# Optimization experiments

Hardware: AMD Instinct MI355X
Metric: run time of the kernel (lower is better)

## Reference

```python
import jax, jax.numpy as jnp
import numpy as np

B = 16384
D = 64            # bottom_mlp_layers[-1] = embedding_dim
DENSE = 512
HIST = 50         # history length per row
C_CAMP = 1000     # num_collisions for campaign table (sqrt(1e6))
C_FEAT = 316      # num_collisions for 1e5-vocab tables
NQ_CAMP = 1000    # ceil(1e6/1000)
NQ_FEAT = 317     # ceil(1e5/316)
NFEAT = 7
N = NFEAT + 1 + 1 # sparse features + dense row
PROJ = 128


def setup_inputs() -> dict:
    key = jax.random.key(0)
    ks = jax.random.split(key, 20)
    inp = {
        'x': jax.random.normal(ks[0], (B, DENSE), jnp.float32),
        'hist_idx': jax.random.randint(ks[1], (B * HIST,), 0, 1000000),
        'hist_offsets': jnp.arange(B, dtype=jnp.int64) * HIST,
        'feat_idx': jax.random.randint(ks[2], (B, NFEAT), 0, 100000),
        # QR embedding tables (quotient, remainder)
        'Wq_c': jax.random.normal(ks[3], (NQ_CAMP, D), jnp.float32) * 0.05,
        'Wr_c': jax.random.normal(ks[4], (C_CAMP, D), jnp.float32) * 0.05,
        'Wq_f': jax.random.normal(ks[5], (NFEAT, NQ_FEAT, D), jnp.float32) * 0.05,
        'Wr_f': jax.random.normal(ks[6], (NFEAT, C_FEAT, D), jnp.float32) * 0.05,
        # bottom MLP: 512->512 relu 512->256 relu 256->64
        'W0': jax.random.normal(ks[7], (512, DENSE), jnp.float32) * 0.03,
        'b0': jnp.zeros((512,), jnp.float32),
        'W1': jax.random.normal(ks[8], (256, 512), jnp.float32) * 0.04,
        'b1': jnp.zeros((256,), jnp.float32),
        'W2': jax.random.normal(ks[9], (64, 256), jnp.float32) * 0.06,
        'b2': jnp.zeros((64,), jnp.float32),
        # projection: (D + (N^2-N)/2) -> PROJ ; 64 + 36 = 100
        'Wp': jax.random.normal(ks[10], (PROJ, D + (N * N - N) // 2), jnp.float32) * 0.1,
        'bp': jnp.zeros((PROJ,), jnp.float32),
    }
    return inp


def _forward(x, hist_idx, hist_offsets, feat_idx, Wq_c, Wr_c, Wq_f, Wr_f,
             W0, b0, W1, b1, W2, b2, Wp, bp):
    # bottom MLP
    h = jax.nn.relu(x @ W0.T + b0)
    h = jax.nn.relu(h @ W1.T + b1)
    dense = h @ W2.T + b2                                   # [B, D]

    # QR embedding bag (mode='mean', operation='mult') for history feature
    e = Wq_c[hist_idx // C_CAMP] * Wr_c[hist_idx % C_CAMP]  # [M, D]
    M = hist_idx.shape[0]
    seg = jnp.cumsum(jnp.zeros((M,), jnp.int32).at[hist_offsets].add(1)) - 1
    sums = jax.ops.segment_sum(e, seg, num_segments=B)      # [B, D]
    counts = jnp.diff(jnp.concatenate([hist_offsets, jnp.array([M], hist_offsets.dtype)]))
    hist_emb = sums / counts[:, None].astype(sums.dtype)

    # single-valued QR lookups (bag size 1 -> mean == lookup)
    t = jnp.arange(NFEAT)[None, :]
    fe = Wq_f[t, feat_idx // C_FEAT] * Wr_f[t, feat_idx % C_FEAT]  # [B, NFEAT, D]

    # pairwise dot interaction: upper triangle (offset=1) of T @ T^T
    T = jnp.concatenate([dense[:, None, :], hist_emb[:, None, :], fe], axis=1)  # [B, N, D]
    Z = jnp.einsum('bnd,bmd->bnm', T, T)
    row, col = np.triu_indices(N, k=1)
    Z_flat = Z[:, row, col]                                  # [B, (N^2-N)/2]

    combined = jnp.concatenate([dense, Z_flat], axis=1)
    return combined @ Wp.T + bp                              # [B, PROJ]


def reference(x, hist_idx, hist_offsets, feat_idx, Wq_c, Wr_c, Wq_f, Wr_f,
              W0, b0, W1, b1, W2, b2, Wp, bp):
    return _forward(x, hist_idx, hist_offsets, feat_idx, Wq_c, Wr_c, Wq_f, Wr_f,
                    W0, b0, W1, b1, W2, b2, Wp, bp)
```

## Files before the change

kernel.cpp:

```cpp
#include <hip/hip_runtime.h>
#include <hip/hip_bf16.h>
#include <stdint.h>

#define DENSE_D 512
#define HIDDEN1 512
#define HIDDEN2 256
#define EMB_D   64
#define NFEAT   7
#define NROWS   9
#define NPAIRS  36
#define COMB    100
#define KPROJ   128
#define PROJ    128
#define C_CAMP  1000
#define C_FEAT  316
#define NQ_FEAT 317
#define TROWS   16

typedef __attribute__((ext_vector_type(8)))  __bf16 bf16x8;
typedef __attribute__((ext_vector_type(8)))  unsigned short ushort8;
typedef __attribute__((ext_vector_type(4)))  float  facc4;

#define GLD_LDS16(gp, lp) __builtin_amdgcn_global_load_lds( \
    (__attribute__((address_space(1))) void*)(gp), \
    (__attribute__((address_space(3))) void*)(lp), 16, 0, 0)

__device__ inline unsigned short f2bf(float f) {
    __hip_bfloat16 h = __float2bfloat16(f);
    return *reinterpret_cast<unsigned short*>(&h);
}
__device__ inline float blo(unsigned int u) { return __uint_as_float(u << 16); }
__device__ inline float bhi(unsigned int u) { return __uint_as_float(u & 0xffff0000u); }

template<int BM, int BN, int BK, bool RELU>
__global__ __launch_bounds__(256)
void gemm16(const unsigned short* __restrict__ A,
            const unsigned short* __restrict__ W,
            const float* __restrict__ bias,
            unsigned short* __restrict__ Cout,
            int M, int N, int K)
{
    constexpr int THREADS = 256;
    constexpr int MREP    = BM / 16;
    constexpr int NREP    = BN / (4 * 16);
    constexpr int SUB     = BK / 32;
    constexpr int ACH     = BM * BK / 8;
    constexpr int BCH     = BN * BK / 8;

    __shared__ __align__(16) unsigned short Asm[BK / 8][BM][8];
    __shared__ __align__(16) unsigned short Bsm[BK / 8][BN][8];

    const int tid  = threadIdx.x;
    const int lane = tid & 63;
    const int wave = tid >> 6;
    const int row0 = blockIdx.x * BM;
    const int col0 = blockIdx.y * BN;
    const int fr   = lane & 15;
    const int fk   = lane >> 4;

    facc4 acc[MREP][NREP] = {};

    for (int k0 = 0; k0 < K; k0 += BK) {
        #pragma unroll
        for (int it = 0; it < ACH / THREADS; ++it) {
            const int p  = it * THREADS + tid;
            const int r  = p & (BM - 1);
            const int kc = p / BM;
            GLD_LDS16(A + (size_t)(row0 + r) * K + k0 + kc * 8,
                      (&Asm[0][0][0]) + (size_t)p * 8);
        }
        #pragma unroll
        for (int it = 0; it < BCH / THREADS; ++it) {
            const int p  = it * THREADS + tid;
            const int r  = p & (BN - 1);
            const int kc = p / BN;
            GLD_LDS16(W + (size_t)(col0 + r) * K + k0 + kc * 8,
                      (&Bsm[0][0][0]) + (size_t)p * 8);
        }
        __syncthreads();

        #pragma unroll
        for (int s = 0; s < SUB; ++s) {
            bf16x8 af[MREP], bw[NREP];
            #pragma unroll
            for (int m = 0; m < MREP; ++m)
                af[m] = *reinterpret_cast<const bf16x8*>(
                    &Asm[s * 4 + fk][m * 16 + fr][0]);
            #pragma unroll
            for (int n = 0; n < NREP; ++n)
                bw[n] = *reinterpret_cast<const bf16x8*>(
                    &Bsm[s * 4 + fk][wave * (NREP * 16) + n * 16 + fr][0]);
            #pragma unroll
            for (int m = 0; m < MREP; ++m)
                #pragma unroll
                for (int n = 0; n < NREP; ++n)
                    acc[m][n] = __builtin_amdgcn_mfma_f32_16x16x32_bf16(
                        af[m], bw[n], acc[m][n], 0, 0, 0);
        }
        __syncthreads();
    }

    #pragma unroll
    for (int n = 0; n < NREP; ++n) {
        const int col = col0 + wave * (NREP * 16) + n * 16 + fr;
        const float bv = bias[col];
        #pragma unroll
        for (int m = 0; m < MREP; ++m) {
            #pragma unroll
            for (int j = 0; j < 4; ++j) {
                const int row = row0 + m * 16 + fk * 4 + j;
                float v = acc[m][n][j] + bv;
                if (RELU) v = fmaxf(v, 0.f);
                Cout[(size_t)row * N + col] = f2bf(v);
            }
        }
    }
}

__device__ inline void cast_seg(const float* __restrict__ src,
                                unsigned short* __restrict__ dst,
                                int n4, int id, int stride)
{
    for (int i = id; i < n4; i += stride) {
        const float4 v = reinterpret_cast<const float4*>(src)[i];
        ushort4 o;
        o.x = f2bf(v.x); o.y = f2bf(v.y); o.z = f2bf(v.z); o.w = f2bf(v.w);
        reinterpret_cast<ushort4*>(dst)[i] = o;
    }
}

__global__ __launch_bounds__(256)
void prep_all(const float* __restrict__ x,
              const float* __restrict__ W0, const float* __restrict__ W1,
              const float* __restrict__ W2, const float* __restrict__ Wp,
              const float* __restrict__ Wq_c, const float* __restrict__ Wr_c,
              const float* __restrict__ Wq_f, const float* __restrict__ Wr_f,
              unsigned short* xb,
              unsigned short* w0b, unsigned short* w1b, unsigned short* w2b,
              unsigned short* wpb, unsigned short* qcb, unsigned short* rcb,
              unsigned short* qfb, unsigned short* rfb, int M)
{
    const int id = blockIdx.x * blockDim.x + threadIdx.x;
    const int stride = gridDim.x * blockDim.x;
    cast_seg(x,    xb,  M * DENSE_D / 4,         id, stride);
    cast_seg(W0,   w0b, HIDDEN1 * DENSE_D / 4,   id, stride);
    cast_seg(W1,   w1b, HIDDEN2 * HIDDEN1 / 4,   id, stride);
    cast_seg(W2,   w2b, EMB_D * HIDDEN2 / 4,     id, stride);
    cast_seg(Wq_c, qcb, C_CAMP * EMB_D / 4,      id, stride);
    cast_seg(Wr_c, rcb, C_CAMP * EMB_D / 4,      id, stride);
    cast_seg(Wq_f, qfb, NFEAT * NQ_FEAT * EMB_D / 4, id, stride);
    cast_seg(Wr_f, rfb, NFEAT * C_FEAT * EMB_D / 4,  id, stride);
    for (int i = id; i < PROJ * KPROJ; i += stride) {
        const int r = i >> 7, c = i & 127;
        wpb[i] = (c < COMB) ? f2bf(Wp[r * COMB + c]) : (unsigned short)0;
    }
}

__global__ __launch_bounds__(256)
void tail_fused(const unsigned short* __restrict__ h1b,
                const unsigned short* __restrict__ w2b,
                const float* __restrict__ b2,
                const int* __restrict__ hist_idx,
                const int* __restrict__ hist_off,
                const int* __restrict__ feat_idx,
                const unsigned short* __restrict__ qcb,
                const unsigned short* __restrict__ rcb,
                const unsigned short* __restrict__ qfb,
                const unsigned short* __restrict__ rfb,
                const unsigned short* __restrict__ wpb,
                const float* __restrict__ bp,
                float* __restrict__ out,
                int B, int Mtot)
{
    const int r0   = blockIdx.x * TROWS;
    const int t    = threadIdx.x;
    const int lane = t & 63;
    const int wave = t >> 6;
    const int fr   = lane & 15;
    const int fk   = lane >> 4;

    __shared__ __align__(16) unsigned short T[TROWS][NROWS][68];
    __shared__ __align__(16) unsigned short combs[TROWS][136];

    {
        facc4 acc = {};
        const unsigned short* arow = h1b + (size_t)(r0 + fr) * HIDDEN2;
        const unsigned short* brow = w2b + (size_t)(wave * 16 + fr) * HIDDEN2;
        #pragma unroll
        for (int kw = 0; kw < 8; ++kw) {
            const bf16x8 af = *reinterpret_cast<const bf16x8*>(arow + kw * 32 + fk * 8);
            const bf16x8 bw = *reinterpret_cast<const bf16x8*>(brow + kw * 32 + fk * 8);
            acc = __builtin_amdgcn_mfma_f32_16x16x32_bf16(af, bw, acc, 0, 0, 0);
        }
        const int col = wave * 16 + fr;
        const float bv = b2[col];
        #pragma unroll
        for (int j = 0; j < 4; ++j) {
            const int row = fk * 4 + j;
            const unsigned short hv = f2bf(acc[j] + bv);
            T[row][0][col]  = hv;
            combs[row][col] = hv;
        }
    }

    for (int p = t; p < TROWS * 18; p += 256) {
        const int row = p / 18, c = p % 18;
        *reinterpret_cast<unsigned int*>(&combs[row][100 + c * 2]) = 0u;
    }

    {
        const int row = t >> 4;
        const int oc  = t & 15;
        const int br  = r0 + row;

        const int fbase = br * NFEAT;
        #pragma unroll
        for (int f = 0; f < NFEAT; ++f) {
            const int fi = feat_idx[fbase + f];
            const int q = fi / C_FEAT, r = fi - q * C_FEAT;
            const uint2 qv = *reinterpret_cast<const uint2*>(
                qfb + ((size_t)f * NQ_FEAT + q) * EMB_D + oc * 4);
            const uint2 rv = *reinterpret_cast<const uint2*>(
                rfb + ((size_t)f * C_FEAT + r) * EMB_D + oc * 4);
            union { ushort4 v; uint2 u; } pk;
            pk.v.x = f2bf(blo(qv.x) * blo(rv.x));
            pk.v.y = f2bf(bhi(qv.x) * bhi(rv.x));
            pk.v.z = f2bf(blo(qv.y) * blo(rv.y));
            pk.v.w = f2bf(bhi(qv.y) * bhi(rv.y));
            *reinterpret_cast<uint2*>(&T[row][2 + f][oc * 4]) = pk.u;
        }

        const int start = hist_off[br];
        const int end   = (br + 1 < B) ? hist_off[br + 1] : Mtot;
        const int cnt   = end - start;
        const int* hp = hist_idx + start;
        float a0 = 0.f, a1 = 0.f, a2 = 0.f, a3 = 0.f;
        #pragma unroll 2
        for (int i = 0; i < cnt; ++i) {
            const int hi = hp[i];
            const int q = hi / C_CAMP, r = hi - q * C_CAMP;
            const uint2 qv = *reinterpret_cast<const uint2*>(qcb + (size_t)q * EMB_D + oc * 4);
            const uint2 rv = *reinterpret_cast<const uint2*>(rcb + (size_t)r * EMB_D + oc * 4);
            a0 += blo(qv.x) * blo(rv.x);
            a1 += bhi(qv.x) * bhi(rv.x);
            a2 += blo(qv.y) * blo(rv.y);
            a3 += bhi(qv.y) * bhi(rv.y);
        }
        const float inv = 1.f / (float)max(cnt, 1);
        union { ushort4 v; uint2 u; } pk;
        pk.v.x = f2bf(a0 * inv); pk.v.y = f2bf(a1 * inv);
        pk.v.z = f2bf(a2 * inv); pk.v.w = f2bf(a3 * inv);
        *reinterpret_cast<uint2*>(&T[row][1][oc * 4]) = pk.u;
    }
    __syncthreads();

    for (int p = t; p < NPAIRS * TROWS; p += 256) {
        const int row = p & (TROWS - 1);
        const int pr  = p / TROWS;
        int i = 0, rem = pr;
        while (rem >= (NROWS - 1) - i) { rem -= (NROWS - 1) - i; ++i; }
        const int j = i + 1 + rem;
        const unsigned short* ti = &T[row][i][0];
        const unsigned short* tj = &T[row][j][0];
        float s = 0.f;
        #pragma unroll
        for (int d = 0; d < EMB_D; d += 4) {
            const uint2 u = *reinterpret_cast<const uint2*>(ti + d);
            const uint2 v = *reinterpret_cast<const uint2*>(tj + d);
            s += blo(u.x) * blo(v.x) + bhi(u.x) * bhi(v.x)
               + blo(u.y) * blo(v.y) + bhi(u.y) * bhi(v.y);
        }
        combs[row][EMB_D + pr] = f2bf(s);
    }
    __syncthreads();

    {
        facc4 acc[2] = {};
        #pragma unroll
        for (int kw = 0; kw < 4; ++kw) {
            const bf16x8 af = *reinterpret_cast<const bf16x8*>(
                &combs[fr][kw * 32 + fk * 8]);
            #pragma unroll
            for (int n = 0; n < 2; ++n) {
                const bf16x8 bw = *reinterpret_cast<const bf16x8*>(
                    wpb + (size_t)(wave * 32 + n * 16 + fr) * KPROJ + kw * 32 + fk * 8);
                acc[n] = __builtin_amdgcn_mfma_f32_16x16x32_bf16(af, bw, acc[n], 0, 0, 0);
            }
        }
        #pragma unroll
        for (int n = 0; n < 2; ++n) {
            const int col = wave * 32 + n * 16 + fr;
            const float bv = bp[col];
            #pragma unroll
            for (int j = 0; j < 4; ++j) {
                const int row = fk * 4 + j;
                out[(size_t)(r0 + row) * PROJ + col] = acc[n][j] + bv;
            }
        }
    }
}

extern "C" void kernel_launch(void* const* d_in, const int* in_sizes, int n_in,
                              void* d_out, int out_size, void* d_ws, size_t ws_size,
                              hipStream_t stream)
{
    const float* x        = (const float*)d_in[0];
    const int*   hist_idx = (const int*)  d_in[1];
    const int*   hist_off = (const int*)  d_in[2];
    const int*   feat_idx = (const int*)  d_in[3];
    const float* Wq_c     = (const float*)d_in[4];
    const float* Wr_c     = (const float*)d_in[5];
    const float* Wq_f     = (const float*)d_in[6];
    const float* Wr_f     = (const float*)d_in[7];
    const float* W0       = (const float*)d_in[8];
    const float* b0       = (const float*)d_in[9];
    const float* W1       = (const float*)d_in[10];
    const float* b1       = (const float*)d_in[11];
    const float* W2       = (const float*)d_in[12];
    const float* b2       = (const float*)d_in[13];
    const float* Wp       = (const float*)d_in[14];
    const float* bp       = (const float*)d_in[15];

    const int M    = in_sizes[0] / DENSE_D;
    const int Mtot = in_sizes[1];

    char* w = (char*)d_ws;
    auto take = [&](size_t bytes) { char* p = w; w += (bytes + 255) & ~(size_t)255; return p; };
    unsigned short* xb  = (unsigned short*)take((size_t)M * DENSE_D * 2);
    unsigned short* w0b = (unsigned short*)take(HIDDEN1 * DENSE_D * 2);
    unsigned short* w1b = (unsigned short*)take(HIDDEN2 * HIDDEN1 * 2);
    unsigned short* w2b = (unsigned short*)take(EMB_D * HIDDEN2 * 2);
    unsigned short* wpb = (unsigned short*)take(PROJ * KPROJ * 2);
    unsigned short* qcb = (unsigned short*)take(C_CAMP * EMB_D * 2);
    unsigned short* rcb = (unsigned short*)take(C_CAMP * EMB_D * 2);
    unsigned short* qfb = (unsigned short*)take(NFEAT * NQ_FEAT * EMB_D * 2);
    unsigned short* rfb = (unsigned short*)take(NFEAT * C_FEAT * EMB_D * 2);
    unsigned short* h0b = (unsigned short*)take((size_t)M * HIDDEN1 * 2);
    unsigned short* h1b = (unsigned short*)take((size_t)M * HIDDEN2 * 2);

    prep_all<<<2048, 256, 0, stream>>>(x, W0, W1, W2, Wp, Wq_c, Wr_c, Wq_f, Wr_f,
                                       xb, w0b, w1b, w2b, wpb, qcb, rcb, qfb, rfb, M);

    gemm16<64, 128, 64, true><<<dim3(M / 64, HIDDEN1 / 128), 256, 0, stream>>>(
        xb, w0b, b0, h0b, M, HIDDEN1, DENSE_D);

    gemm16<64, 128, 64, true><<<dim3(M / 64, HIDDEN2 / 128), 256, 0, stream>>>(
        h0b, w1b, b1, h1b, M, HIDDEN2, HIDDEN1);

    tail_fused<<<M / TROWS, 256, 0, stream>>>(
        h1b, w2b, b2, hist_idx, hist_off, feat_idx,
        qcb, rcb, qfb, rfb, wpb, bp, (float*)d_out, M, Mtot);
}
```

Baseline: 93.61 us.

## Fuse fp32-to-bf16 cast of x into first GEMM, retile it, prestage history offsets

Drops the separate cast of x to bf16 in the prep kernel. The first GEMM now loads fp32 x directly, converts it in registers and stores it to LDS, which saves a full write and re-read of the bf16 copy of x. That GEMM is retiled to 128x128 with a 2x2 wave layout and BK=32. The history embedding loop precomputes quotient/remainder offsets into shared memory so the dependent-load loop no longer does integer division. The trade-off is that the fp32 A path loses the async global_load_lds and adds register conversion work. HISTMAX=52 also silently assumes every bag holds at most 52 entries.

Result: faster. 85.07 us (-9.1%).

```diff
diff --git a/kernel.cpp b/kernel.cpp
--- a/kernel.cpp
+++ b/kernel.cpp
@@ -16,6 +16,7 @@
 #define C_FEAT  316
 #define NQ_FEAT 317
 #define TROWS   16
+#define HISTMAX 52
 
 typedef __attribute__((ext_vector_type(8)))  __bf16 bf16x8;
 typedef __attribute__((ext_vector_type(8)))  unsigned short ushort8;
@@ -32,17 +33,17 @@
 __device__ inline float blo(unsigned int u) { return __uint_as_float(u << 16); }
 __device__ inline float bhi(unsigned int u) { return __uint_as_float(u & 0xffff0000u); }
 
-template<int BM, int BN, int BK, bool RELU>
-__global__ __launch_bounds__(256)
-void gemm16(const unsigned short* __restrict__ A,
+template<int BM, int BN, int BK, int WM, int WN, bool RELU, bool A_F32>
+__global__ __launch_bounds__(WM * WN * 64)
+void gemm16(const void* __restrict__ Avoid,
             const unsigned short* __restrict__ W,
             const float* __restrict__ bias,
             unsigned short* __restrict__ Cout,
             int M, int N, int K)
 {
-    constexpr int THREADS = 256;
-    constexpr int MREP    = BM / 16;
-    constexpr int NREP    = BN / (4 * 16);
+    constexpr int THREADS = WM * WN * 64;
+    constexpr int MREP    = BM / (WM * 16);
+    constexpr int NREP    = BN / (WN * 16);
     constexpr int SUB     = BK / 32;
     constexpr int ACH     = BM * BK / 8;
     constexpr int BCH     = BN * BK / 8;
@@ -53,6 +54,8 @@
     const int tid  = threadIdx.x;
     const int lane = tid & 63;
     const int wave = tid >> 6;
+    const int wm   = wave / WN;
+    const int wn   = wave % WN;
     const int row0 = blockIdx.x * BM;
     const int col0 = blockIdx.y * BN;
     const int fr   = lane & 15;
@@ -61,13 +64,34 @@
     facc4 acc[MREP][NREP] = {};
 
     for (int k0 = 0; k0 < K; k0 += BK) {
-        #pragma unroll
-        for (int it = 0; it < ACH / THREADS; ++it) {
-            const int p  = it * THREADS + tid;
-            const int r  = p & (BM - 1);
-            const int kc = p / BM;
-            GLD_LDS16(A + (size_t)(row0 + r) * K + k0 + kc * 8,
-                      (&Asm[0][0][0]) + (size_t)p * 8);
+        if (A_F32) {
+            const float* Af = (const float*)Avoid;
+            #pragma unroll
+            for (int it = 0; it < ACH / THREADS; ++it) {
+                const int p  = it * THREADS + tid;
+                const int r  = p & (BM - 1);
+                const int kc = p / BM;
+                const float* src = Af + (size_t)(row0 + r) * K + k0 + kc * 8;
+                const float4 v0 = *reinterpret_cast<const float4*>(src);
+                const float4 v1 = *reinterpret_cast<const float4*>(src + 4);
+                ushort8 cv;
+                cv[0] = f2bf(v0.x); cv[1] = f2bf(v0.y);
+                cv[2] = f2bf(v0.z); cv[3] = f2bf(v0.w);
+                cv[4] = f2bf(v1.x); cv[5] = f2bf(v1.y);
+                cv[6] = f2bf(v1.z); cv[7] = f2bf(v1.w);
+                *reinterpret_cast<ushort8*>(
+                    (unsigned short*)(&Asm[0][0][0]) + (size_t)p * 8) = cv;
+            }
+        } else {
+            const unsigned short* Ab = (const unsigned short*)Avoid;
+            #pragma unroll
+            for (int it = 0; it < ACH / THREADS; ++it) {
+                const int p  = it * THREADS + tid;
+                const int r  = p & (BM - 1);
+                const int kc = p / BM;
+                GLD_LDS16(Ab + (size_t)(row0 + r) * K + k0 + kc * 8,
+                          (&Asm[0][0][0]) + (size_t)p * 8);
+            }
         }
         #pragma unroll
         for (int it = 0; it < BCH / THREADS; ++it) {
@@ -85,11 +109,11 @@
             #pragma unroll
             for (int m = 0; m < MREP; ++m)
                 af[m] = *reinterpret_cast<const bf16x8*>(
-                    &Asm[s * 4 + fk][m * 16 + fr][0]);
+                    &Asm[s * 4 + fk][wm * (MREP * 16) + m * 16 + fr][0]);
             #pragma unroll
             for (int n = 0; n < NREP; ++n)
                 bw[n] = *reinterpret_cast<const bf16x8*>(
-                    &Bsm[s * 4 + fk][wave * (NREP * 16) + n * 16 + fr][0]);
+                    &Bsm[s * 4 + fk][wn * (NREP * 16) + n * 16 + fr][0]);
             #pragma unroll
             for (int m = 0; m < MREP; ++m)
                 #pragma unroll
@@ -102,13 +126,13 @@
 
     #pragma unroll
     for (int n = 0; n < NREP; ++n) {
-        const int col = col0 + wave * (NREP * 16) + n * 16 + fr;
+        const int col = col0 + wn * (NREP * 16) + n * 16 + fr;
         const float bv = bias[col];
         #pragma unroll
         for (int m = 0; m < MREP; ++m) {
             #pragma unroll
             for (int j = 0; j < 4; ++j) {
-                const int row = row0 + m * 16 + fk * 4 + j;
+                const int row = row0 + wm * (MREP * 16) + m * 16 + fk * 4 + j;
                 float v = acc[m][n][j] + bv;
                 if (RELU) v = fmaxf(v, 0.f);
                 Cout[(size_t)row * N + col] = f2bf(v);
@@ -130,19 +154,16 @@
 }
 
 __global__ __launch_bounds__(256)
-void prep_all(const float* __restrict__ x,
-              const float* __restrict__ W0, const float* __restrict__ W1,
+void prep_all(const float* __restrict__ W0, const float* __restrict__ W1,
               const float* __restrict__ W2, const float* __restrict__ Wp,
               const float* __restrict__ Wq_c, const float* __restrict__ Wr_c,
               const float* __restrict__ Wq_f, const float* __restrict__ Wr_f,
-              unsigned short* xb,
               unsigned short* w0b, unsigned short* w1b, unsigned short* w2b,
               unsigned short* wpb, unsigned short* qcb, unsigned short* rcb,
-              unsigned short* qfb, unsigned short* rfb, int M)
+              unsigned short* qfb, unsigned short* rfb)
 {
     const int id = blockIdx.x * blockDim.x + threadIdx.x;
     const int stride = gridDim.x * blockDim.x;
-    cast_seg(x,    xb,  M * DENSE_D / 4,         id, stride);
     cast_seg(W0,   w0b, HIDDEN1 * DENSE_D / 4,   id, stride);
     cast_seg(W1,   w1b, HIDDEN2 * HIDDEN1 / 4,   id, stride);
     cast_seg(W2,   w2b, EMB_D * HIDDEN2 / 4,     id, stride);
@@ -181,6 +202,7 @@
 
     __shared__ __align__(16) unsigned short T[TROWS][NROWS][68];
     __shared__ __align__(16) unsigned short combs[TROWS][136];
+    __shared__ int2 soff[TROWS][HISTMAX];
 
     {
         facc4 acc = {};
@@ -234,13 +256,20 @@
         const int end   = (br + 1 < B) ? hist_off[br + 1] : Mtot;
         const int cnt   = end - start;
         const int* hp = hist_idx + start;
+        for (int i = oc; i < cnt; i += 16) {
+            const int hi = hp[i];
+            const int q = hi / C_CAMP;
+            soff[row][i] = make_int2(q * EMB_D, (hi - q * C_CAMP) * EMB_D);
+        }
+
+        const unsigned short* qb = qcb + oc * 4;
+        const unsigned short* rb = rcb + oc * 4;
         float a0 = 0.f, a1 = 0.f, a2 = 0.f, a3 = 0.f;
         #pragma unroll 2
         for (int i = 0; i < cnt; ++i) {
-            const int hi = hp[i];
-            const int q = hi / C_CAMP, r = hi - q * C_CAMP;
-            const uint2 qv = *reinterpret_cast<const uint2*>(qcb + (size_t)q * EMB_D + oc * 4);
-            const uint2 rv = *reinterpret_cast<const uint2*>(rcb + (size_t)r * EMB_D + oc * 4);
+            const int2 o = soff[row][i];
+            const uint2 qv = *reinterpret_cast<const uint2*>(qb + o.x);
+            const uint2 rv = *reinterpret_cast<const uint2*>(rb + o.y);
             a0 += blo(qv.x) * blo(rv.x);
             a1 += bhi(qv.x) * bhi(rv.x);
             a2 += blo(qv.y) * blo(rv.y);
@@ -326,7 +355,6 @@
 
     char* w = (char*)d_ws;
     auto take = [&](size_t bytes) { char* p = w; w += (bytes + 255) & ~(size_t)255; return p; };
-    unsigned short* xb  = (unsigned short*)take((size_t)M * DENSE_D * 2);
     unsigned short* w0b = (unsigned short*)take(HIDDEN1 * DENSE_D * 2);
     unsigned short* w1b = (unsigned short*)take(HIDDEN2 * HIDDEN1 * 2);
     unsigned short* w2b = (unsigned short*)take(EMB_D * HIDDEN2 * 2);
@@ -338,13 +366,15 @@
     unsigned short* h0b = (unsigned short*)take((size_t)M * HIDDEN1 * 2);
     unsigned short* h1b = (unsigned short*)take((size_t)M * HIDDEN2 * 2);
 
-    prep_all<<<2048, 256, 0, stream>>>(x, W0, W1, W2, Wp, Wq_c, Wr_c, Wq_f, Wr_f,
-                                       xb, w0b, w1b, w2b, wpb, qcb, rcb, qfb, rfb, M);
-
-    gemm16<64, 128, 64, true><<<dim3(M / 64, HIDDEN1 / 128), 256, 0, stream>>>(
-        xb, w0b, b0, h0b, M, HIDDEN1, DENSE_D);
-
-    gemm16<64, 128, 64, true><<<dim3(M / 64, HIDDEN2 / 128), 256, 0, stream>>>(
+    prep_all<<<256, 256, 0, stream>>>(W0, W1, W2, Wp, Wq_c, Wr_c, Wq_f, Wr_f,
+                                      w0b, w1b, w2b, wpb, qcb, rcb, qfb, rfb);
+
+    gemm16<128, 128, 32, 2, 2, true, true>
+        <<<dim3(M / 128, HIDDEN1 / 128), 256, 0, stream>>>(
+        x, w0b, b0, h0b, M, HIDDEN1, DENSE_D);
+
+    gemm16<64, 128, 64, 1, 4, true, false>
+        <<<dim3(M / 64, HIDDEN2 / 128), 256, 0, stream>>>(
         h0b, w1b, b1, h1b, M, HIDDEN2, HIDDEN1);
 
     tail_fused<<<M / TROWS, 256, 0, stream>>>(
```
